# Kernel tuning notes

Measured on AMD Instinct MI355X. Metric: run time of the kernel, lower is better.

Reference implementation:

```python
import jax, jax.numpy as jnp
import numpy as np

B, T, F, H = 64, 512, 132, 1024


def setup_inputs() -> dict:
    key = jax.random.key(0)
    ks = jax.random.split(key, 16)
    k = 1.0 / np.sqrt(H)
    u = lambda kk, shape: jax.random.uniform(kk, shape, jnp.float32, -k, k)
    return {
        "real_seq": jax.random.normal(ks[0], (B, T, F), jnp.float32),
        "Wih1": u(ks[1], (4 * H, F)), "Whh1": u(ks[2], (4 * H, H)),
        "bih1": u(ks[3], (4 * H,)), "bhh1": u(ks[4], (4 * H,)),
        "Wih2": u(ks[5], (4 * H, H)), "Whh2": u(ks[6], (4 * H, H)),
        "bih2": u(ks[7], (4 * H,)), "bhh2": u(ks[8], (4 * H,)),
        "Wih3": u(ks[9], (4 * H, H)), "Whh3": u(ks[10], (4 * H, H)),
        "bih3": u(ks[11], (4 * H,)), "bhh3": u(ks[12], (4 * H,)),
        "Wd": u(ks[13], (F, H)), "bd": u(ks[14], (F,)),
        "condition_num": 5, "groundtruth_num": 5,
    }


def _cell(x, h, c, Wih, Whh, bih, bhh):
    # torch LSTMCell gate order: i, f, g, o
    gates = x @ Wih.T + h @ Whh.T + bih + bhh
    i, f, g, o = jnp.split(gates, 4, axis=-1)
    c_new = jax.nn.sigmoid(f) * c + jax.nn.sigmoid(i) * jnp.tanh(g)
    h_new = jax.nn.sigmoid(o) * jnp.tanh(c_new)
    return h_new, c_new


def reference(real_seq, Wih1, Whh1, bih1, bhh1, Wih2, Whh2, bih2, bhh2,
              Wih3, Whh3, bih3, bhh3, Wd, bd, condition_num, groundtruth_num):
    batch, seq_len, _ = real_seq.shape
    hid = Whh1.shape[1]
    out_dim = Wd.shape[0]
    # static teacher-forcing schedule (numpy, as in get_condition_lst)
    gt = np.ones((100, groundtruth_num))
    con = np.zeros((100, condition_num))
    cond = jnp.asarray(np.concatenate((gt, con), 1).reshape(-1)[:seq_len],
                       jnp.float32)

    def step(carry, xs):
        h0, h1, h2, c0, c1, c2, prev_out = carry
        frame, flag = xs
        in_frame = jnp.where(flag == 1.0, frame, prev_out)
        # NOTE: faithful to source -- lstm2 gets OLD h0, lstm3 gets OLD h1
        h0n, c0n = _cell(in_frame, h0, c0, Wih1, Whh1, bih1, bhh1)
        h1n, c1n = _cell(h0, h1, c1, Wih2, Whh2, bih2, bhh2)
        h2n, c2n = _cell(h1, h2, c2, Wih3, Whh3, bih3, bhh3)
        out = h2n @ Wd.T + bd
        return (h0n, h1n, h2n, c0n, c1n, c2n, out), out

    z = jnp.zeros((batch, hid), real_seq.dtype)
    out0 = jnp.zeros((batch, out_dim), real_seq.dtype)
    _, outs = jax.lax.scan(step, (z, z, z, z, z, z, out0),
                           (jnp.swapaxes(real_seq, 0, 1), cond))
    # outs: [T, B, F] -> concat along feature axis per timestep: [B, T*F]
    return jnp.transpose(outs, (1, 0, 2)).reshape(batch, seq_len * out_dim)
```

## Files before the change

kernel.cpp:

```cpp
#include <hip/hip_runtime.h>
#include <cstdint>


#define NBLK 256
#define NTHR 512
#define Bn 64
#define Tn 512
#define Fn 132
#define Hn 1024
#define TF (Tn * Fn)
#define SRCH 65536
#define HBUF 196608
#define XTT 10240
#define WPB 102400
#define STB 393216

typedef _Float16 h8 __attribute__((ext_vector_type(8)));
typedef float f4 __attribute__((ext_vector_type(4)));
typedef int v4i __attribute__((ext_vector_type(4)));
typedef unsigned long long ull;

__device__ v4i llvm_amdgcn_raw_buffer_load_v4i32(v4i srsrc, int voffset,
                                                 int soffset, int aux)
    __asm("llvm.amdgcn.raw.buffer.load.v4i32");

__device__ __forceinline__ v4i make_srd(const void* p) {
    union { struct { unsigned lo, hi, sz, cfg; } s; v4i v; } u;
    u.s.lo = (unsigned)(uintptr_t)p;
    u.s.hi = (unsigned)((uintptr_t)p >> 32);
    u.s.sz = 0xFFFFFFFFu;
    u.s.cfg = 0x00020000u;
    return u.v;
}

__device__ __forceinline__ h8 bload16(v4i rsrc, int voff) {
    union { v4i i; h8 h; } c;
    c.i = llvm_amdgcn_raw_buffer_load_v4i32(rsrc, voff, 0, 1 );
    return c.h;
}

__device__ __forceinline__ float sigf(float x) { return 1.0f / (1.0f + expf(-x)); }

__device__ __forceinline__ ull cload8(const void* p) {
    return __hip_atomic_load((const ull*)p, __ATOMIC_RELAXED, __HIP_MEMORY_SCOPE_AGENT);
}
__device__ __forceinline__ void cstore8(void* p, ull v) {
    __hip_atomic_store((ull*)p, v, __ATOMIC_RELAXED, __HIP_MEMORY_SCOPE_AGENT);
}

__device__ __forceinline__ void garrive(unsigned* bar, unsigned ep) {
    unsigned* cnt = bar + ((blockIdx.x >> 5) << 5);
    unsigned old = __hip_atomic_fetch_add(cnt, 1u, __ATOMIC_RELAXED,
                                          __HIP_MEMORY_SCOPE_AGENT);
    if (old == 32u * ep - 1u) {
        unsigned d = __hip_atomic_fetch_add(bar + 256, 1u, __ATOMIC_RELAXED,
                                            __HIP_MEMORY_SCOPE_AGENT);
        if (d == 8u * ep - 1u)
            __hip_atomic_store(bar + 288, ep, __ATOMIC_RELAXED,
                               __HIP_MEMORY_SCOPE_AGENT);
    }
}
__device__ __forceinline__ void gwait(unsigned* bar, unsigned ep) {
    while (__hip_atomic_load(bar + 288, __ATOMIC_RELAXED,
                             __HIP_MEMORY_SCOPE_AGENT) < ep)
        __builtin_amdgcn_s_sleep(1);
}
__device__ __forceinline__ void gsyncA(unsigned* bar, unsigned ep) {
    __syncthreads();
    if (threadIdx.x == 0) { garrive(bar, ep); gwait(bar, ep); }
    __syncthreads();
}


__global__ void k_bsum(const float* bih1, const float* bhh1, const float* bih2,
                       const float* bhh2, const float* bih3, const float* bhh3,
                       const float* Wih1, const float* bd,
                       float* bsum, float* bsum2) {
    int i = blockIdx.x * 256 + threadIdx.x;
    if (i < NBLK * 48) {
        int bidw = i / 48, r = i % 48;
        int cell = r >> 4, n = r & 15;
        int row = (n >> 2) * Hn + bidw * 4 + (n & 3);
        const float* bi = cell == 0 ? bih1 : (cell == 1 ? bih2 : bih3);
        const float* bh = cell == 0 ? bhh1 : (cell == 1 ? bhh2 : bhh3);
        bsum[i] = bi[row] + bh[row];
    } else if (i < NBLK * 64) {
        int ii = i - NBLK * 48;
        int bidw = ii / 16, n = ii % 16;
        int row = (n >> 2) * Hn + bidw * 4 + (n & 3);
        float s = 0.0f;
        for (int f = 0; f < Fn; ++f) s += Wih1[(size_t)row * Fn + f] * bd[f];
        bsum2[bidw * 16 + n] = s;
    }
}

__global__ void k_convx(const float* xseq, _Float16* xT) {
    int i = blockIdx.x * 256 + threadIdx.x;
    if (i >= Tn * XTT) return;
    int t = i / XTT, r = i % XTT;
    int k8 = r >> 9, b = (r >> 3) & 63, e = r & 7;
    int f = k8 * 8 + e;
    float v = (f < Fn) ? xseq[((size_t)b * Tn + t) * Fn + f] : 0.0f;
    xT[i] = (_Float16)v;
}

__global__ void k_convw(const float* Wih1, const float* Whh1, const float* Wih2,
                        const float* Whh2, const float* Wih3, const float* Whh3,
                        const float* Wd, _Float16* wblob) {
    int i = blockIdx.x * 256 + threadIdx.x;
    if (i >= NBLK * WPB) return;
    int bidw = i / WPB, r = i % WPB;
    int slot = r >> 9, e = r & 511;
    int w = slot / 25, s = slot - w * 25;
    int l = e >> 3, j = e & 7;
    int kq = l >> 4, n = l & 15;
    int row = (n >> 2) * Hn + bidw * 4 + (n & 3);
    float v = 0.0f;
    if (s >= 21) {
        int kt = w * 4 + (s - 21);
        int k = kt * 32 + kq * 8 + j;
        float acc = 0.0f;
        for (int f = 0; f < Fn; ++f)
            acc += Wih1[(size_t)row * Fn + f] * Wd[(size_t)f * Hn + k];
        v = acc;
    } else {
        const float* M;
        int K, kt;
        if (s < 4)       { M = Whh1; K = Hn; kt = w * 4 + s; }
        else if (s < 8)  { M = Wih2; K = Hn; kt = w * 4 + s - 4; }
        else if (s < 12) { M = Whh2; K = Hn; kt = w * 4 + s - 8; }
        else if (s < 16) { M = Wih3; K = Hn; kt = w * 4 + s - 12; }
        else if (s < 20) { M = Whh3; K = Hn; kt = w * 4 + s - 16; }
        else             { M = Wih1; K = Fn; kt = w; }
        int k = kt * 32 + kq * 8 + j;
        if (!(s == 20 && w >= 5) && k < K) v = M[(size_t)row * K + k];
    }
    wblob[i] = (_Float16)v;
}

__global__ void k_misc(_Float16* hT) {
    int i = blockIdx.x * 256 + threadIdx.x;
    if (i < HBUF) hT[i] = (_Float16)0.0f;
}


__global__ __launch_bounds__(NTHR, 1) void lstm_mfma(
    const _Float16* __restrict__ xT, const _Float16* __restrict__ wblob,
    _Float16* __restrict__ hT, unsigned char* __restrict__ xstage,
    const float* __restrict__ bsum, const float* __restrict__ bsum2,
    const float* __restrict__ Wd, const float* __restrict__ bd,
    const int* __restrict__ cnum_p, const int* __restrict__ gnum_p,
    float* __restrict__ dout, unsigned* __restrict__ bar) {
    __shared__ float red[8 * 12 * 68 * 4];
    __shared__ float cst[768];
    __shared__ float sbias[48];
    __shared__ float sbias2[16];
    __shared__ unsigned long long hstage[192];
    __shared__ int sxi[3];

    const int tid = threadIdx.x;
    const int bid = blockIdx.x;
    const int lane = tid & 63;
    const int wid = tid >> 6;
    const int laneAB = (lane >> 4) * 1024 + (lane & 15) * 16;
    const int laneA0 = (lane >> 4) * 512 + (lane & 15) * 8;
    const int widB = wid * 16384;

    if (tid < 48) sbias[tid] = bsum[bid * 48 + tid];
    if (tid >= 64 && tid < 80) sbias2[tid - 64] = bsum2[bid * 16 + (tid - 64)];
    for (int i = tid; i < 768; i += NTHR) cst[i] = 0.0f;

    h8 wfr[25];
    {
        const _Float16* wp = wblob + (size_t)bid * WPB + (size_t)(wid * 25) * 512 + lane * 8;
#pragma unroll
        for (int s2 = 0; s2 < 25; ++s2) wfr[s2] = *(const h8*)(wp + s2 * 512);
    }

    if (tid == 0) {
        unsigned x;
        asm volatile("s_getreg_b32 %0, hwreg(HW_REG_XCC_ID)" : "=s"(x));
        x &= 7u;
        unsigned r = __hip_atomic_fetch_add(bar + 384 + x * 16, 1u,
                                            __ATOMIC_RELAXED, __HIP_MEMORY_SCOPE_AGENT);
        sxi[0] = (int)x; sxi[1] = (int)r;
    }
    gsyncA(bar, 1);
    if (tid == 0)
        sxi[2] = (int)__hip_atomic_load(bar + 384 + sxi[0] * 16, __ATOMIC_RELAXED,
                                        __HIP_MEMORY_SCOPE_AGENT);
    __syncthreads();
    const int xcd = sxi[0], xrank = sxi[1], xN = sxi[2];
    unsigned* xb = bar + 640 + xcd * 16;
    unsigned char* xsb = xstage + (size_t)xcd * 2 * STB;

    const int gnum = gnum_p[0];
    const int per = gnum + cnum_p[0];

    auto decoder = [&](v4i rsrc, int tt) {
        const int ss = tid >> 6, b = tid & 63;
        const int nj = (bid < 8) ? 2 : 1;
        for (int j2 = 0; j2 < nj; ++j2) {
            int f, half;
            if (j2 == 0) {
                if (bid < Fn) { f = bid; half = 0; }
                else          { f = bid - Fn; half = 1; }
            } else { f = bid + (NBLK - Fn); half = 1; }
            const float* wdr = Wd + (size_t)f * Hn;
            h8 hv[8];
#pragma unroll
            for (int i = 0; i < 8; ++i) {
                const int k8 = half * 64 + ss * 8 + i;
                hv[i] = bload16(rsrc, 262144 + k8 * 1024 + b * 16);
            }
            float p = 0.0f;
#pragma unroll
            for (int i = 0; i < 8; ++i) {
                const int k8 = half * 64 + ss * 8 + i;
                const float4 w0 = *(const float4*)(wdr + k8 * 8);
                const float4 w1 = *(const float4*)(wdr + k8 * 8 + 4);
                p = fmaf((float)hv[i][0], w0.x, p); p = fmaf((float)hv[i][1], w0.y, p);
                p = fmaf((float)hv[i][2], w0.z, p); p = fmaf((float)hv[i][3], w0.w, p);
                p = fmaf((float)hv[i][4], w1.x, p); p = fmaf((float)hv[i][5], w1.y, p);
                p = fmaf((float)hv[i][6], w1.z, p); p = fmaf((float)hv[i][7], w1.w, p);
            }
            red[ss * 64 + b] = p;
            __syncthreads();
            if (tid < 64) {
                float o = (half == 0) ? bd[f] : 0.0f;
#pragma unroll
                for (int u = 0; u < 8; ++u) o += red[u * 64 + tid];
                unsafeAtomicAdd(&dout[(size_t)tid * TF + (size_t)tt * Fn + f], o);
            }
            __syncthreads();
        }
    };

    auto stageT = [&](int rbuf, int slot) {
        const ull* src = (const ull*)(hT + (size_t)rbuf * HBUF);
        ull* dst = (ull*)(xsb + (size_t)slot * STB);
        for (int s2 = xrank; s2 < 32; s2 += xN) {
            const int u = s2 * 1536 + tid;
#pragma unroll
            for (int q = 0; q < 3; ++q)
                dst[u + q * 512] = cload8(src + u + q * 512);
        }
        __syncthreads();
    };
    auto xarrive = [&]() {
        if (tid == 0)
            __hip_atomic_fetch_add(xb, 1u, __ATOMIC_RELAXED, __HIP_MEMORY_SCOPE_AGENT);
    };
    auto xpoll = [&](unsigned target) {
        if (tid == 0)
            while (__hip_atomic_load(xb, __ATOMIC_RELAXED, __HIP_MEMORY_SCOPE_AGENT) < target)
                __builtin_amdgcn_s_sleep(1);
        __syncthreads();
    };

    int tmod = 0;
    for (int t = 0; t < Tn; ++t) {
        const int flag = (tmod < gnum) ? 1 : 0;
        const bool fused = (!flag) && (t > 0);
        const int rb = t % 3, wb2 = (t + 1) % 3;
        _Float16* hw = hT + (size_t)wb2 * HBUF;

        const ull* ssrc = (const ull*)(hT + (size_t)rb * HBUF);
        ull* sdst = (ull*)(xsb + (size_t)(t & 1) * STB);
        ull sv0 = 0, sv1 = 0, sv2 = 0;
        int u0 = -1;
        if (xrank < 32) {
            u0 = xrank * 1536 + tid;
            sv0 = cload8(ssrc + u0);
            sv1 = cload8(ssrc + u0 + 512);
            sv2 = cload8(ssrc + u0 + 1024);
        }
        f4 acc[12];
#pragma unroll
        for (int i = 0; i < 12; ++i) acc[i] = (f4){0.f, 0.f, 0.f, 0.f};
        if (u0 >= 0) { sdst[u0] = sv0; sdst[u0 + 512] = sv1; sdst[u0 + 1024] = sv2; }
        for (int s2 = xrank + xN; s2 < 32; s2 += xN) {
            const int u = s2 * 1536 + tid;
#pragma unroll
            for (int q = 0; q < 3; ++q)
                sdst[u + q * 512] = cload8(ssrc + u + q * 512);
        }
        __syncthreads();
        xarrive();

        if (flag && wid < 5) {
            const _Float16* x0 = xT + (size_t)t * XTT + wid * 2048 + laneA0;
            h8 xa[4];
#pragma unroll
            for (int mt = 0; mt < 4; ++mt) xa[mt] = *(const h8*)(x0 + mt * 128);
#pragma unroll
            for (int mt = 0; mt < 4; ++mt)
                acc[mt] = __builtin_amdgcn_mfma_f32_16x16x32_f16(xa[mt], wfr[20], acc[mt], 0, 0, 0);
        }
        xpoll((unsigned)(xN * (t + 1)));
        const v4i rsrc = make_srd(xsb + (size_t)(t & 1) * STB);

        {
            h8 a[16];
#pragma unroll
            for (int i2 = 0; i2 < 4; ++i2)
#pragma unroll
                for (int mt = 0; mt < 4; ++mt)
                    a[i2 * 4 + mt] = bload16(rsrc, widB + i2 * 4096 + mt * 256 + laneAB);
#pragma unroll
            for (int i2 = 0; i2 < 4; ++i2)
#pragma unroll
                for (int mt = 0; mt < 4; ++mt) {
                    acc[mt]     = __builtin_amdgcn_mfma_f32_16x16x32_f16(a[i2 * 4 + mt], wfr[i2],     acc[mt],     0, 0, 0);
                    acc[4 + mt] = __builtin_amdgcn_mfma_f32_16x16x32_f16(a[i2 * 4 + mt], wfr[4 + i2], acc[4 + mt], 0, 0, 0);
                }
        }
        {
            h8 a[16];
#pragma unroll
            for (int i2 = 0; i2 < 4; ++i2)
#pragma unroll
                for (int mt = 0; mt < 4; ++mt)
                    a[i2 * 4 + mt] = bload16(rsrc, 131072 + widB + i2 * 4096 + mt * 256 + laneAB);
#pragma unroll
            for (int i2 = 0; i2 < 4; ++i2)
#pragma unroll
                for (int mt = 0; mt < 4; ++mt) {
                    acc[4 + mt] = __builtin_amdgcn_mfma_f32_16x16x32_f16(a[i2 * 4 + mt], wfr[8 + i2],  acc[4 + mt], 0, 0, 0);
                    acc[8 + mt] = __builtin_amdgcn_mfma_f32_16x16x32_f16(a[i2 * 4 + mt], wfr[12 + i2], acc[8 + mt], 0, 0, 0);
                }
        }
        {
            h8 a[16];
#pragma unroll
            for (int i2 = 0; i2 < 4; ++i2)
#pragma unroll
                for (int mt = 0; mt < 4; ++mt)
                    a[i2 * 4 + mt] = bload16(rsrc, 262144 + widB + i2 * 4096 + mt * 256 + laneAB);
            if (fused) {
#pragma unroll
                for (int i2 = 0; i2 < 4; ++i2)
#pragma unroll
                    for (int mt = 0; mt < 4; ++mt) {
                        acc[8 + mt] = __builtin_amdgcn_mfma_f32_16x16x32_f16(a[i2 * 4 + mt], wfr[16 + i2], acc[8 + mt], 0, 0, 0);
                        acc[mt]     = __builtin_amdgcn_mfma_f32_16x16x32_f16(a[i2 * 4 + mt], wfr[21 + i2], acc[mt],     0, 0, 0);
                    }
            } else {
#pragma unroll
                for (int i2 = 0; i2 < 4; ++i2)
#pragma unroll
                    for (int mt = 0; mt < 4; ++mt)
                        acc[8 + mt] = __builtin_amdgcn_mfma_f32_16x16x32_f16(a[i2 * 4 + mt], wfr[16 + i2], acc[8 + mt], 0, 0, 0);
            }
        }

        {
            float* wr = red + ((size_t)(wid * 12) * 68 + (lane >> 4) * 17 + (lane & 15)) * 4;
#pragma unroll
            for (int cc = 0; cc < 3; ++cc)
#pragma unroll
                for (int mt = 0; mt < 4; ++mt)
                    *(f4*)(wr + (cc * 4 + mt) * 68 * 4) = acc[cc * 4 + mt];
        }
        __syncthreads();
        const float bmul = fused ? 1.0f : 0.0f;
        for (int idx = tid; idx < 768; idx += NTHR) {
            const int cell = idx >> 8, jj = (idx >> 6) & 3, b = idx & 63;
            const int mt = b >> 4, mq = (b >> 2) & 3, rr = b & 3;
            float gv4[4];
#pragma unroll
            for (int gt = 0; gt < 4; ++gt) {
                const int n = gt * 4 + jj;
                float v = sbias[cell * 16 + n];
                if (cell == 0) v += bmul * sbias2[n];
#pragma unroll
                for (int w2 = 0; w2 < 8; ++w2)
                    v += red[(((w2 * 12 + cell * 4 + mt)) * 68 + mq * 17 + n) * 4 + rr];
                gv4[gt] = v;
            }
            const float cold = cst[(cell * 4 + jj) * 64 + b];
            const float cn = sigf(gv4[1]) * cold + sigf(gv4[0]) * tanhf(gv4[2]);
            cst[(cell * 4 + jj) * 64 + b] = cn;
            const float hn = sigf(gv4[3]) * tanhf(cn);
            ((_Float16*)hstage)[(cell * 64 + b) * 4 + jj] = (_Float16)hn;
        }
        __syncthreads();
        if (tid < 192) {
            const int cell = tid >> 6, b = tid & 63;
            _Float16* dst = hw + cell * SRCH + (bid >> 1) * 512 + b * 8 + 4 * (bid & 1);
            cstore8(dst, hstage[tid]);
        }

        __syncthreads();
        if (tid == 0) garrive(bar, (unsigned)(t + 2));
        if (t > 0) decoder(rsrc, t - 1);
        __syncthreads();
        if (tid == 0) gwait(bar, (unsigned)(t + 2));
        __syncthreads();

        tmod = (tmod + 1 >= per) ? 0 : (tmod + 1);
    }

    stageT(Tn % 3, Tn & 1);
    if (tid == 0) {
        __hip_atomic_fetch_add(xb, 1u, __ATOMIC_RELAXED, __HIP_MEMORY_SCOPE_AGENT);
        while (__hip_atomic_load(xb, __ATOMIC_RELAXED, __HIP_MEMORY_SCOPE_AGENT)
               < (unsigned)(xN * (Tn + 1)))
            __builtin_amdgcn_s_sleep(1);
    }
    __syncthreads();
    decoder(make_srd(xsb + (size_t)(Tn & 1) * STB), Tn - 1);
}


extern "C" void kernel_launch(void* const* d_in, const int* in_sizes, int n_in,
                              void* d_out, int out_size, void* d_ws, size_t ws_size,
                              hipStream_t stream) {
    const float* xseq = (const float*)d_in[0];
    const float* Wih1 = (const float*)d_in[1];
    const float* Whh1 = (const float*)d_in[2];
    const float* bih1 = (const float*)d_in[3];
    const float* bhh1 = (const float*)d_in[4];
    const float* Wih2 = (const float*)d_in[5];
    const float* Whh2 = (const float*)d_in[6];
    const float* bih2 = (const float*)d_in[7];
    const float* bhh2 = (const float*)d_in[8];
    const float* Wih3 = (const float*)d_in[9];
    const float* Whh3 = (const float*)d_in[10];
    const float* bih3 = (const float*)d_in[11];
    const float* bhh3 = (const float*)d_in[12];
    const float* Wd = (const float*)d_in[13];
    const float* bd = (const float*)d_in[14];
    const int* cnum_p = (const int*)d_in[15];
    const int* gnum_p = (const int*)d_in[16];

    unsigned char* ws = (unsigned char*)d_ws;
    unsigned* bar = (unsigned*)ws;
    float* bsum = (float*)(ws + 4096);
    float* bsum2 = (float*)(ws + 53248);
    _Float16* xT = (_Float16*)(ws + 102400);
    _Float16* wblob = (_Float16*)(ws + 102400 + 10485760);
    _Float16* hT = (_Float16*)(ws + 102400 + 10485760 + 52428800);
    unsigned char* xstage = ws + 102400 + 10485760 + 52428800 + 1179648;

    hipMemsetAsync(bar, 0, 4096, stream);
    hipMemsetAsync(d_out, 0, (size_t)out_size * sizeof(float), stream);
    hipLaunchKernelGGL(k_bsum, dim3((NBLK * 64 + 255) / 256), dim3(256), 0, stream,
                       bih1, bhh1, bih2, bhh2, bih3, bhh3, Wih1, bd, bsum, bsum2);
    hipLaunchKernelGGL(k_convx, dim3((Tn * XTT + 255) / 256), dim3(256), 0, stream,
                       xseq, xT);
    hipLaunchKernelGGL(k_convw, dim3((NBLK * WPB + 255) / 256), dim3(256), 0, stream,
                       Wih1, Whh1, Wih2, Whh2, Wih3, Whh3, Wd, wblob);
    hipLaunchKernelGGL(k_misc, dim3((HBUF + 255) / 256), dim3(256), 0, stream, hT);
    hipLaunchKernelGGL(lstm_mfma, dim3(NBLK), dim3(NTHR), 0, stream,
                       xT, wblob, hT, xstage, bsum, bsum2, Wd, bd, cnum_p, gnum_p,
                       (float*)d_out, bar);
}
```

Measured before the change: 7.973 ms.

## Replace atomic-counter grid barriers with per-block flag arrays polled by a wavefront

Replaces the hierarchical fetch-add counter barrier, both grid-wide and per-XCD, with per-block epoch flags. Each block stores its epoch to its own slot, and one wavefront polls all slots with vector loads and a wave-wide all-reduce. This removes contended atomic read-modify-write chains and the serialized two-level release on every timestep. In exchange, every poll reads 256 slots, which may add memory traffic, and correctness depends on relaxed stores becoming visible before the data is read.

```diff
diff --git a/kernel.cpp b/kernel.cpp
--- a/kernel.cpp
+++ b/kernel.cpp
@@ -47,28 +47,8 @@
 __device__ __forceinline__ void cstore8(void* p, ull v) {
     __hip_atomic_store((ull*)p, v, __ATOMIC_RELAXED, __HIP_MEMORY_SCOPE_AGENT);
 }
-
-__device__ __forceinline__ void garrive(unsigned* bar, unsigned ep) {
-    unsigned* cnt = bar + ((blockIdx.x >> 5) << 5);
-    unsigned old = __hip_atomic_fetch_add(cnt, 1u, __ATOMIC_RELAXED,
-                                          __HIP_MEMORY_SCOPE_AGENT);
-    if (old == 32u * ep - 1u) {
-        unsigned d = __hip_atomic_fetch_add(bar + 256, 1u, __ATOMIC_RELAXED,
-                                            __HIP_MEMORY_SCOPE_AGENT);
-        if (d == 8u * ep - 1u)
-            __hip_atomic_store(bar + 288, ep, __ATOMIC_RELAXED,
-                               __HIP_MEMORY_SCOPE_AGENT);
-    }
-}
-__device__ __forceinline__ void gwait(unsigned* bar, unsigned ep) {
-    while (__hip_atomic_load(bar + 288, __ATOMIC_RELAXED,
-                             __HIP_MEMORY_SCOPE_AGENT) < ep)
-        __builtin_amdgcn_s_sleep(1);
-}
-__device__ __forceinline__ void gsyncA(unsigned* bar, unsigned ep) {
-    __syncthreads();
-    if (threadIdx.x == 0) { garrive(bar, ep); gwait(bar, ep); }
-    __syncthreads();
+__device__ __forceinline__ void cstore4(unsigned* p, unsigned v) {
+    __hip_atomic_store(p, v, __ATOMIC_RELAXED, __HIP_MEMORY_SCOPE_AGENT);
 }
 
 
@@ -177,6 +157,24 @@
         for (int s2 = 0; s2 < 25; ++s2) wfr[s2] = *(const h8*)(wp + s2 * 512);
     }
 
+    auto gArrive = [&](unsigned ep) {
+        if (tid == 0) cstore4(bar + bid, ep);
+    };
+    auto gPoll = [&](unsigned ep) {
+        if (tid < 64) {
+            const ull* p = (const ull*)bar;
+            for (;;) {
+                ull a = cload8(p + lane);
+                ull b = cload8(p + 64 + lane);
+                bool ok = ((unsigned)a >= ep) & ((unsigned)(a >> 32) >= ep) &
+                          ((unsigned)b >= ep) & ((unsigned)(b >> 32) >= ep);
+                if (__all((int)ok)) break;
+                __builtin_amdgcn_s_sleep(2);
+            }
+        }
+        __syncthreads();
+    };
+
     if (tid == 0) {
         unsigned x;
         asm volatile("s_getreg_b32 %0, hwreg(HW_REG_XCC_ID)" : "=s"(x));
@@ -185,17 +183,41 @@
                                             __ATOMIC_RELAXED, __HIP_MEMORY_SCOPE_AGENT);
         sxi[0] = (int)x; sxi[1] = (int)r;
     }
-    gsyncA(bar, 1);
+    __syncthreads();
+    gArrive(1u);
+    gPoll(1u);
     if (tid == 0)
         sxi[2] = (int)__hip_atomic_load(bar + 384 + sxi[0] * 16, __ATOMIC_RELAXED,
                                         __HIP_MEMORY_SCOPE_AGENT);
     __syncthreads();
     const int xcd = sxi[0], xrank = sxi[1], xN = sxi[2];
-    unsigned* xb = bar + 640 + xcd * 16;
+    const int nst = (xN < 32) ? xN : 32;
+    unsigned* xsl = bar + 512 + xcd * 64;
     unsigned char* xsb = xstage + (size_t)xcd * 2 * STB;
 
     const int gnum = gnum_p[0];
     const int per = gnum + cnum_p[0];
+
+    auto xArrive = [&](unsigned ver) {
+        if (tid == 0 && xrank < 32) cstore4(xsl + xrank, ver);
+    };
+    auto xPoll = [&](unsigned ver) {
+        if (tid < 64) {
+            const ull* p = (const ull*)xsl;
+            for (;;) {
+                bool ok = true;
+                if (lane < 16) {
+                    ull a = cload8(p + lane);
+                    const int s0 = lane * 2, s1 = s0 + 1;
+                    ok = (s0 >= nst || (unsigned)a >= ver) &&
+                         (s1 >= nst || (unsigned)(a >> 32) >= ver);
+                }
+                if (__all((int)ok)) break;
+                __builtin_amdgcn_s_sleep(2);
+            }
+        }
+        __syncthreads();
+    };
 
     auto decoder = [&](v4i rsrc, int tt) {
         const int ss = tid >> 6, b = tid & 63;
@@ -236,28 +258,6 @@
         }
     };
 
-    auto stageT = [&](int rbuf, int slot) {
-        const ull* src = (const ull*)(hT + (size_t)rbuf * HBUF);
-        ull* dst = (ull*)(xsb + (size_t)slot * STB);
-        for (int s2 = xrank; s2 < 32; s2 += xN) {
-            const int u = s2 * 1536 + tid;
-#pragma unroll
-            for (int q = 0; q < 3; ++q)
-                dst[u + q * 512] = cload8(src + u + q * 512);
-        }
-        __syncthreads();
-    };
-    auto xarrive = [&]() {
-        if (tid == 0)
-            __hip_atomic_fetch_add(xb, 1u, __ATOMIC_RELAXED, __HIP_MEMORY_SCOPE_AGENT);
-    };
-    auto xpoll = [&](unsigned target) {
-        if (tid == 0)
-            while (__hip_atomic_load(xb, __ATOMIC_RELAXED, __HIP_MEMORY_SCOPE_AGENT) < target)
-                __builtin_amdgcn_s_sleep(1);
-        __syncthreads();
-    };
-
     int tmod = 0;
     for (int t = 0; t < Tn; ++t) {
         const int flag = (tmod < gnum) ? 1 : 0;
@@ -286,7 +286,7 @@
                 sdst[u + q * 512] = cload8(ssrc + u + q * 512);
         }
         __syncthreads();
-        xarrive();
+        xArrive((unsigned)(t + 1));
 
         if (flag && wid < 5) {
             const _Float16* x0 = xT + (size_t)t * XTT + wid * 2048 + laneA0;
@@ -297,7 +297,7 @@
             for (int mt = 0; mt < 4; ++mt)
                 acc[mt] = __builtin_amdgcn_mfma_f32_16x16x32_f16(xa[mt], wfr[20], acc[mt], 0, 0, 0);
         }
-        xpoll((unsigned)(xN * (t + 1)));
+        xPoll((unsigned)(t + 1));
         const v4i rsrc = make_srd(xsb + (size_t)(t & 1) * STB);
 
         {
@@ -392,24 +392,28 @@
         }
 
         __syncthreads();
-        if (tid == 0) garrive(bar, (unsigned)(t + 2));
+        gArrive((unsigned)(t + 2));
         if (t > 0) decoder(rsrc, t - 1);
         __syncthreads();
-        if (tid == 0) gwait(bar, (unsigned)(t + 2));
-        __syncthreads();
+        gPoll((unsigned)(t + 2));
 
         tmod = (tmod + 1 >= per) ? 0 : (tmod + 1);
     }
 
-    stageT(Tn % 3, Tn & 1);
-    if (tid == 0) {
-        __hip_atomic_fetch_add(xb, 1u, __ATOMIC_RELAXED, __HIP_MEMORY_SCOPE_AGENT);
-        while (__hip_atomic_load(xb, __ATOMIC_RELAXED, __HIP_MEMORY_SCOPE_AGENT)
-               < (unsigned)(xN * (Tn + 1)))
-            __builtin_amdgcn_s_sleep(1);
-    }
-    __syncthreads();
-    decoder(make_srd(xsb + (size_t)(Tn & 1) * STB), Tn - 1);
+    {
+        const ull* ssrc = (const ull*)(hT + (size_t)(Tn % 3) * HBUF);
+        ull* sdst = (ull*)(xsb + (size_t)(Tn & 1) * STB);
+        for (int s2 = xrank; s2 < 32; s2 += xN) {
+            const int u = s2 * 1536 + tid;
+#pragma unroll
+            for (int q = 0; q < 3; ++q)
+                sdst[u + q * 512] = cload8(ssrc + u + q * 512);
+        }
+        __syncthreads();
+        xArrive((unsigned)(Tn + 1));
+        xPoll((unsigned)(Tn + 1));
+        decoder(make_srd(xsb + (size_t)(Tn & 1) * STB), Tn - 1);
+    }
 }
 
 
```

Result: slower. 9.191 ms (+15.3%).
